# Performance work log

Measured on AMD Instinct MI355X. Metric: run time of the kernel, lower is better.

## Reference

```python
import jax, jax.numpy as jnp
import numpy as np


def setup_inputs() -> dict:
    key = jax.random.key(0)
    kq, kk, kv = jax.random.split(key, 3)
    B, Nq, Nk, d = 16, 4096, 4096, 128
    return {
        "query": jax.random.normal(kq, (B, Nq, d), dtype=jnp.float32),
        "key": jax.random.normal(kk, (B, Nk, d), dtype=jnp.float32),
        "value": jax.random.normal(kv, (B, Nk, d), dtype=jnp.float32),
    }


def reference(query, key, value):
    # weights = softmax(QK^T / sqrt(d)) with causal mask; dropout p=0.0 is identity
    d = key.shape[-1]
    scale = 1.0 / jnp.sqrt(jnp.asarray(d, dtype=query.dtype))
    scores = jnp.einsum("bqd,bkd->bqk", query, key) * scale  # [B, Nq, Nk]
    Nq, Nk = scores.shape[-2], scores.shape[-1]
    causal = jnp.tril(jnp.ones((Nq, Nk), dtype=bool))
    scores = jnp.where(causal, scores, jnp.asarray(-jnp.inf, dtype=scores.dtype))
    weights = jax.nn.softmax(scores, axis=-1)
    return jnp.einsum("bqk,bkv->bqv", weights, value)
```

## Files before the change

kernel.cpp:

```cpp
#include <hip/hip_runtime.h>
#include <stdint.h>


#define NB 16
#define NS 4096
#define DH 128

typedef float          fx4   __attribute__((ext_vector_type(4)));
typedef uint32_t       ux4   __attribute__((ext_vector_type(4)));
typedef __bf16         bfv8  __attribute__((ext_vector_type(8)));
typedef __bf16         bfv4  __attribute__((ext_vector_type(4)));
typedef unsigned short u16x4 __attribute__((ext_vector_type(4)));

typedef const uint32_t __attribute__((address_space(1))) glob_u32;
typedef uint32_t       __attribute__((address_space(3))) lds_u32;

__device__ __forceinline__ fx4 mfma16(bfv8 a, bfv8 b, fx4 c) {
  return __builtin_amdgcn_mfma_f32_16x16x32_bf16(a, b, c, 0, 0, 0);
}

__global__ void __launch_bounds__(256) prepack_kernel(
    const float* __restrict__ K, const float* __restrict__ V,
    unsigned short* __restrict__ Kf, unsigned short* __restrict__ Vf) {
  __shared__ __align__(16) unsigned short tile[64][136];
  const int bid = blockIdx.x;
  const int b = bid >> 6, kvblk = bid & 63;
  const int kvb = kvblk << 6;
  const int tid = threadIdx.x;
  const size_t fbase = ((size_t)(b * 64 + kvblk)) * 8192;

  {
    const int tt = tid >> 6, lane = tid & 63;
    const int ln16 = lane & 15, g = lane >> 4;
    const float* kp = K + (((size_t)(b * NS + kvb + 16 * tt + ln16)) << 7) + 8 * g;
    unsigned short* op = Kf + fbase + tt * 2048 + lane * 8;
#pragma unroll
    for (int c = 0; c < 4; ++c) {
      fx4 a0 = *(const fx4*)(kp + 32 * c);
      fx4 a1 = *(const fx4*)(kp + 32 * c + 4);
      bfv8 t;
#pragma unroll
      for (int j = 0; j < 4; ++j) {
        t[j]     = (__bf16)a0[j];
        t[j + 4] = (__bf16)a1[j];
      }
      *(ux4*)(op + c * 512) = __builtin_bit_cast(ux4, t);
    }
  }

  {
    const int r = tid >> 2, cq = tid & 3;
    const float* vp = V + (((size_t)(b * NS + kvb + r)) << 7) + 32 * cq;
#pragma unroll
    for (int h = 0; h < 4; ++h) {
      fx4 f0 = *(const fx4*)(vp + 8 * h);
      fx4 f1 = *(const fx4*)(vp + 8 * h + 4);
      bfv8 t;
#pragma unroll
      for (int j = 0; j < 4; ++j) {
        t[j]     = (__bf16)f0[j];
        t[j + 4] = (__bf16)f1[j];
      }
      *(ux4*)&tile[r][32 * cq + 8 * h] = __builtin_bit_cast(ux4, t);
    }
  }
  __syncthreads();
  {
    const int dt = tid >> 5, c = (tid >> 4) & 1, ln16 = tid & 15;
    const int d = 16 * dt + ln16;
    unsigned short* op = Vf + fbase + c * 4096 + dt * 512 + ln16 * 8;
#pragma unroll
    for (int g = 0; g < 4; ++g) {
      unsigned short e[8];
#pragma unroll
      for (int j = 0; j < 4; ++j) {
        e[j]     = tile[32 * c + 4 * g + j][d];
        e[j + 4] = tile[32 * c + 16 + 4 * g + j][d];
      }
      *(ux4*)(op + g * 128) = *(const ux4*)e;
    }
  }
}

__global__ void __launch_bounds__(512, 4) attn_kernel(
    const float* __restrict__ Q, const unsigned short* __restrict__ Kf,
    const unsigned short* __restrict__ Vf, float* __restrict__ O,
    unsigned short* __restrict__ Pa, float* __restrict__ Ml, int split) {
  __shared__ __align__(16) unsigned char sm[32768];

  const int wid  = blockIdx.x;
  const int tid  = threadIdx.x;
  const int w    = tid >> 6;
  const int lane = tid & 63;
  const int g    = lane >> 4;
  const int ln16 = lane & 15;

  int b, t, u0, un, mode;
  int t1 = 0, u1b = 0;
  int again = 0;

  if (split) {
    const int piece = wid >> 8;
    const int v     = (wid >> 4) & 15;
    b = wid & 15;
    t = 31 - v;
    if (piece == 0) {
      u0 = 0; un = 66; mode = 1;
    } else {
      u0 = 66; un = 128 - 4 * v; mode = 2;
      t1 = v; u1b = 4 * v + 4; again = 1;
    }
  } else {
    const int half = wid >> 8, ii = wid & 255;
    b = ii & 15;
    const int qi = ii >> 4;
    t = half ? qi : 31 - qi;
    u0 = 0; un = 4 * t + 4; mode = 0;
  }

  const float SCALE = 0.12753102f;
  const fx4 z4 = {0.f, 0.f, 0.f, 0.f};

  const unsigned char* kfB = (const unsigned char*)Kf + (size_t)b * 1048576;
  const unsigned char* vfB = (const unsigned char*)Vf + (size_t)b * 1048576;

#define STAGE(jb, bo)                                                         \
  do {                                                                        \
    const unsigned char* gk = kfB + (size_t)(jb) * 8192;                      \
    const unsigned char* gv = vfB + (size_t)(jb) * 8192;                      \
    __builtin_amdgcn_global_load_lds((glob_u32*)(gk + w * 1024 + lane * 16),  \
                                     (lds_u32*)(sm + (bo) + w * 1024), 16, 0, 0); \
    __builtin_amdgcn_global_load_lds((glob_u32*)(gv + w * 1024 + lane * 16),  \
                                     (lds_u32*)(sm + (bo) + 8192 + w * 1024), 16, 0, 0); \
  } while (0)

  for (;;) {
    const int qw = (t << 7) + 16 * w;

    bfv8 qf[4];
#pragma unroll
    for (int c = 0; c < 4; ++c) {
      const float* qp = Q + (((size_t)(b * NS + qw + ln16)) << 7) + 32 * c + 8 * g;
      fx4 a0 = *(const fx4*)qp;
      fx4 a1 = *(const fx4*)(qp + 4);
      bfv8 tt_;
#pragma unroll
      for (int j = 0; j < 4; ++j) {
        tt_[j]     = (__bf16)(a0[j] * SCALE);
        tt_[j + 4] = (__bf16)(a1[j] * SCALE);
      }
      qf[c] = tt_;
    }

    fx4 acc[8];
#pragma unroll
    for (int dt = 0; dt < 8; ++dt) acc[dt] = z4;
    float mrun = -1e30f;
    float lsum = 0.f;

    const int nkvw = (qw >> 5) + 1;
    const int qrow = qw + ln16;

    STAGE(u0, 0);
    asm volatile("s_waitcnt vmcnt(0)" ::: "memory");
    __builtin_amdgcn_s_barrier();
    asm volatile("" ::: "memory");

    int cur = 0;
    for (int jb = u0; jb < un; ++jb) {
      if (jb + 1 < un) STAGE(jb + 1, (cur ^ 1) * 16384);

      if (jb < nkvw) {
        const unsigned char* kb = sm + cur * 16384;
        const unsigned char* vb = kb + 8192;

        fx4 s[2];
        s[0] = z4; s[1] = z4;
        __builtin_amdgcn_s_setprio(1);
#pragma unroll
        for (int tt = 0; tt < 2; ++tt) {
#pragma unroll
          for (int c = 0; c < 4; ++c) {
            bfv8 kfr = *(const bfv8*)(kb + tt * 4096 + c * 1024 + lane * 16);
            s[tt] = mfma16(kfr, qf[c], s[tt]);
          }
        }
        __builtin_amdgcn_s_setprio(0);

        const int kvb = jb << 5;
        if (kvb + 31 > qrow - ln16 + 0 + (qw - qw) + qw - qw + qw % 1 + 31 * 0 + (qw & 0) ? (kvb + 31 > qw) : 0) {  }
        if (kvb + 31 > qw) {
#pragma unroll
          for (int tt = 0; tt < 2; ++tt)
#pragma unroll
            for (int r = 0; r < 4; ++r) {
              int kvpos = kvb + 16 * tt + 4 * g + r;
              if (kvpos > qrow) s[tt][r] = -1e30f;
            }
        }

        fx4 m4 = __builtin_elementwise_max(s[0], s[1]);
        float pm = fmaxf(fmaxf(m4[0], m4[1]), fmaxf(m4[2], m4[3]));
        pm = fmaxf(pm, __shfl_xor(pm, 16));
        pm = fmaxf(pm, __shfl_xor(pm, 32));
        if (__any(pm > mrun + 8.0f)) {
          float mn = fmaxf(mrun, pm);
          float f  = __builtin_amdgcn_exp2f(mrun - mn);
          lsum *= f;
#pragma unroll
          for (int dt = 0; dt < 8; ++dt) acc[dt] *= f;
          mrun = mn;
        }
#pragma unroll
        for (int tt = 0; tt < 2; ++tt)
#pragma unroll
          for (int r = 0; r < 4; ++r)
            s[tt][r] = __builtin_amdgcn_exp2f(s[tt][r] - mrun);
        fx4 r4 = s[0] + s[1];
        float rs = (r4[0] + r4[1]) + (r4[2] + r4[3]);
        rs += __shfl_xor(rs, 16);
        rs += __shfl_xor(rs, 32);
        lsum += rs;
        bfv8 pb;
#pragma unroll
        for (int j = 0; j < 4; ++j) {
          pb[j]     = (__bf16)s[0][j];
          pb[j + 4] = (__bf16)s[1][j];
        }

        __builtin_amdgcn_s_setprio(1);
#pragma unroll
        for (int dt = 0; dt < 8; ++dt) {
          bfv8 vfr = *(const bfv8*)(vb + dt * 1024 + lane * 16);
          acc[dt] = mfma16(vfr, pb, acc[dt]);
        }
        __builtin_amdgcn_s_setprio(0);
      }

      asm volatile("s_waitcnt vmcnt(0)" ::: "memory");
      __builtin_amdgcn_s_barrier();
      asm volatile("" ::: "memory");
      cur ^= 1;
    }

    if (mode == 0) {
      float inv = 1.0f / lsum;
      float* ob = O + (((size_t)(b * NS + qrow)) << 7) + 4 * g;
#pragma unroll
      for (int dt = 0; dt < 8; ++dt) *(fx4*)(ob + 16 * dt) = acc[dt] * inv;
    } else {
      if (mode == 1) {
        float* ob = O + (((size_t)(b * NS + qrow)) << 7) + 4 * g;
#pragma unroll
        for (int dt = 0; dt < 8; ++dt) *(fx4*)(ob + 16 * dt) = acc[dt];
      } else {
        const int row = 16 * w + ln16;
        unsigned short* pp =
            Pa + (((size_t)((b * 16 + (t - 16)) * 128 + row)) << 7) + 4 * g;
#pragma unroll
        for (int dt = 0; dt < 8; ++dt) {
          bfv4 t4;
#pragma unroll
          for (int j = 0; j < 4; ++j) t4[j] = (__bf16)acc[dt][j];
          *(u16x4*)(pp + 16 * dt) = __builtin_bit_cast(u16x4, t4);
        }
      }
      if (g == 0) {
        const int slot = mode - 1;
        const int row = 16 * w + ln16;
        float* mlp = Ml + (size_t)(((b * 16 + (t - 16)) * 2 + slot) * 2) * 128;
        mlp[row]       = mrun;
        mlp[128 + row] = lsum;
      }
    }

    if (!again) break;
    again = 0;
    t = t1; u0 = 0; un = u1b; mode = 0;
  }
#undef STAGE
}

__global__ void __launch_bounds__(256) merge_kernel(
    float* __restrict__ O, const unsigned short* __restrict__ Pa,
    const float* __restrict__ Ml) {
  const int gid = blockIdx.x * 256 + threadIdx.x;
  const int d4  = gid & 31;
  const int rg  = gid >> 5;
  const int b   = rg >> 11;
  const int r2  = rg & 2047;
  const int tt  = r2 >> 7;
  const int row = r2 & 127;

  const float* mlp = Ml + (size_t)((b * 16 + tt) * 4) * 128;
  const float m1 = mlp[row],       l1 = mlp[128 + row];
  const float m2 = mlp[256 + row], l2 = mlp[384 + row];
  const float m  = fmaxf(m1, m2);
  const float w1 = __builtin_amdgcn_exp2f(m1 - m);
  const float w2 = __builtin_amdgcn_exp2f(m2 - m);

  float* op = O + (((size_t)(b * NS + (16 + tt) * 128 + row)) << 7) + 4 * d4;
  fx4 a1 = *(const fx4*)op;
  const unsigned short* pp =
      Pa + (((size_t)((b * 16 + tt) * 128 + row)) << 7) + 4 * d4;
  bfv4 a2b = __builtin_bit_cast(bfv4, *(const u16x4*)pp);
  fx4 a2;
#pragma unroll
  for (int j = 0; j < 4; ++j) a2[j] = (float)a2b[j];

  const float inv = 1.0f / (w1 * l1 + w2 * l2);
  fx4 o = (a1 * w1 + a2 * w2) * inv;
  *(fx4*)op = o;
}

extern "C" void kernel_launch(void* const* d_in, const int* in_sizes, int n_in,
                              void* d_out, int out_size, void* d_ws, size_t ws_size,
                              hipStream_t stream) {
  (void)in_sizes; (void)n_in; (void)out_size;
  const float* Q = (const float*)d_in[0];
  const float* K = (const float*)d_in[1];
  const float* V = (const float*)d_in[2];
  float* O = (float*)d_out;

  unsigned short* Kf = (unsigned short*)d_ws;
  unsigned short* Vf = Kf + (size_t)NB * NS * DH;
  unsigned short* Pa = (unsigned short*)((char*)d_ws + 33554432);
  float*          Ml = (float*)((char*)d_ws + 41943040);

  const size_t NEED = 41943040 + 524288;
  const int split = (ws_size >= NEED) ? 1 : 0;

  prepack_kernel<<<dim3(NB * 64), dim3(256), 0, stream>>>(K, V, Kf, Vf);
  attn_kernel<<<dim3(512), dim3(512), 0, stream>>>(Q, Kf, Vf, O, Pa, Ml, split);
  if (split) merge_kernel<<<dim3(4096), dim3(256), 0, stream>>>(O, Pa, Ml);
}
```

Baseline: 124.5 us.

## Give each wave two query tiles and stage four KV blocks per barrier

The block drops from 8 to 4 waves, and each wave now handles 32 query rows as two 16-row tiles, so every K/V fragment read from LDS feeds two MFMAs. K/V staging now loads four 32-key blocks per batch into 64KB of LDS, paying one barrier and wait per four blocks instead of one per block. The split point of the two-piece split changes from 66 to 64. In exchange, register pressure roughly doubles, fewer waves are resident, and the load is no longer overlapped with compute: each batch waits for all four blocks to arrive.

```diff
diff --git a/kernel.cpp b/kernel.cpp
--- a/kernel.cpp
+++ b/kernel.cpp
@@ -82,11 +82,11 @@
   }
 }
 
-__global__ void __launch_bounds__(512, 4) attn_kernel(
+__global__ void __launch_bounds__(256, 2) attn_kernel(
     const float* __restrict__ Q, const unsigned short* __restrict__ Kf,
     const unsigned short* __restrict__ Vf, float* __restrict__ O,
     unsigned short* __restrict__ Pa, float* __restrict__ Ml, int split) {
-  __shared__ __align__(16) unsigned char sm[32768];
+  __shared__ __align__(16) unsigned char sm[65536];
 
   const int wid  = blockIdx.x;
   const int tid  = threadIdx.x;
@@ -96,18 +96,17 @@
   const int ln16 = lane & 15;
 
   int b, t, u0, un, mode;
-  int t1 = 0, u1b = 0;
-  int again = 0;
+  int t1 = 0, u1b = 0, again = 0;
 
   if (split) {
-    const int piece = wid >> 8;
-    const int v     = (wid >> 4) & 15;
+    const int half = wid >> 8;
+    const int v    = (wid >> 4) & 15;
     b = wid & 15;
     t = 31 - v;
-    if (piece == 0) {
-      u0 = 0; un = 66; mode = 1;
+    if (half == 0) {
+      u0 = 0; un = 64; mode = 1;
     } else {
-      u0 = 66; un = 128 - 4 * v; mode = 2;
+      u0 = 64; un = 128 - 4 * v; mode = 2;
       t1 = v; u1b = 4 * v + 4; again = 1;
     }
   } else {
@@ -124,153 +123,198 @@
   const unsigned char* kfB = (const unsigned char*)Kf + (size_t)b * 1048576;
   const unsigned char* vfB = (const unsigned char*)Vf + (size_t)b * 1048576;
 
-#define STAGE(jb, bo)                                                         \
-  do {                                                                        \
-    const unsigned char* gk = kfB + (size_t)(jb) * 8192;                      \
-    const unsigned char* gv = vfB + (size_t)(jb) * 8192;                      \
-    __builtin_amdgcn_global_load_lds((glob_u32*)(gk + w * 1024 + lane * 16),  \
-                                     (lds_u32*)(sm + (bo) + w * 1024), 16, 0, 0); \
-    __builtin_amdgcn_global_load_lds((glob_u32*)(gv + w * 1024 + lane * 16),  \
-                                     (lds_u32*)(sm + (bo) + 8192 + w * 1024), 16, 0, 0); \
+#define STAGE(jb, so)                                                          \
+  do {                                                                         \
+    const unsigned char* gk = kfB + (size_t)(jb) * 8192;                       \
+    const unsigned char* gv = vfB + (size_t)(jb) * 8192;                       \
+    __builtin_amdgcn_global_load_lds((glob_u32*)(gk + w * 2048 + lane * 16),   \
+        (lds_u32*)(sm + (so) + w * 2048), 16, 0, 0);                           \
+    __builtin_amdgcn_global_load_lds((glob_u32*)(gk + w * 2048 + 1024 + lane * 16), \
+        (lds_u32*)(sm + (so) + w * 2048 + 1024), 16, 0, 0);                    \
+    __builtin_amdgcn_global_load_lds((glob_u32*)(gv + w * 2048 + lane * 16),   \
+        (lds_u32*)(sm + (so) + 8192 + w * 2048), 16, 0, 0);                    \
+    __builtin_amdgcn_global_load_lds((glob_u32*)(gv + w * 2048 + 1024 + lane * 16), \
+        (lds_u32*)(sm + (so) + 8192 + w * 2048 + 1024), 16, 0, 0);             \
   } while (0)
 
+#define COMPUTE(jb, so)                                                        \
+  do {                                                                         \
+    const unsigned char* kb = sm + (so);                                       \
+    const unsigned char* vb = kb + 8192;                                       \
+    fx4 s[2][2];                                                               \
+    s[0][0] = z4; s[0][1] = z4; s[1][0] = z4; s[1][1] = z4;                    \
+    __builtin_amdgcn_s_setprio(1);                                             \
+    _Pragma("unroll")                                                          \
+    for (int tt = 0; tt < 2; ++tt) {                                           \
+      _Pragma("unroll")                                                        \
+      for (int c = 0; c < 4; ++c) {                                            \
+        bfv8 kfr = *(const bfv8*)(kb + tt * 4096 + c * 1024 + lane * 16);      \
+        s[0][tt] = mfma16(kfr, qf[0][c], s[0][tt]);                            \
+        s[1][tt] = mfma16(kfr, qf[1][c], s[1][tt]);                            \
+      }                                                                        \
+    }                                                                          \
+    __builtin_amdgcn_s_setprio(0);                                             \
+    const int kvb = (jb) << 5;                                                 \
+    if (kvb + 31 > qw) {                                                       \
+      _Pragma("unroll")                                                        \
+      for (int qt = 0; qt < 2; ++qt) {                                         \
+        const int qrow = qw + qt * 16 + ln16;                                  \
+        _Pragma("unroll")                                                      \
+        for (int tt = 0; tt < 2; ++tt)                                         \
+          _Pragma("unroll")                                                    \
+          for (int r = 0; r < 4; ++r) {                                        \
+            int kvpos = kvb + 16 * tt + 4 * g + r;                             \
+            if (kvpos > qrow) s[qt][tt][r] = -1e30f;                           \
+          }                                                                    \
+      }                                                                        \
+    }                                                                          \
+    bfv8 pb[2];                                                                \
+    _Pragma("unroll")                                                          \
+    for (int qt = 0; qt < 2; ++qt) {                                           \
+      fx4 m4 = __builtin_elementwise_max(s[qt][0], s[qt][1]);                  \
+      float pm = fmaxf(fmaxf(m4[0], m4[1]), fmaxf(m4[2], m4[3]));              \
+      pm = fmaxf(pm, __shfl_xor(pm, 16));                                      \
+      pm = fmaxf(pm, __shfl_xor(pm, 32));                                      \
+      if (__any(pm > mrun[qt] + 8.0f)) {                                       \
+        float mn = fmaxf(mrun[qt], pm);                                        \
+        float f  = __builtin_amdgcn_exp2f(mrun[qt] - mn);                      \
+        lsum[qt] *= f;                                                         \
+        _Pragma("unroll")                                                      \
+        for (int dt = 0; dt < 8; ++dt) acc[qt][dt] *= f;                       \
+        mrun[qt] = mn;                                                         \
+      }                                                                        \
+      _Pragma("unroll")                                                        \
+      for (int tt = 0; tt < 2; ++tt)                                           \
+        _Pragma("unroll")                                                      \
+        for (int r = 0; r < 4; ++r)                                            \
+          s[qt][tt][r] = __builtin_amdgcn_exp2f(s[qt][tt][r] - mrun[qt]);      \
+      fx4 r4 = s[qt][0] + s[qt][1];                                            \
+      float rs = (r4[0] + r4[1]) + (r4[2] + r4[3]);                            \
+      rs += __shfl_xor(rs, 16);                                                \
+      rs += __shfl_xor(rs, 32);                                                \
+      lsum[qt] += rs;                                                          \
+      bfv8 tt_;                                                                \
+      _Pragma("unroll")                                                        \
+      for (int j = 0; j < 4; ++j) {                                            \
+        tt_[j]     = (__bf16)s[qt][0][j];                                      \
+        tt_[j + 4] = (__bf16)s[qt][1][j];                                      \
+      }                                                                        \
+      pb[qt] = tt_;                                                            \
+    }                                                                          \
+    __builtin_amdgcn_s_setprio(1);                                             \
+    _Pragma("unroll")                                                          \
+    for (int dt = 0; dt < 8; ++dt) {                                           \
+      bfv8 vfr = *(const bfv8*)(vb + dt * 1024 + lane * 16);                   \
+      acc[0][dt] = mfma16(vfr, pb[0], acc[0][dt]);                             \
+      acc[1][dt] = mfma16(vfr, pb[1], acc[1][dt]);                             \
+    }                                                                          \
+    __builtin_amdgcn_s_setprio(0);                                             \
+  } while (0)
+
   for (;;) {
-    const int qw = (t << 7) + 16 * w;
-
-    bfv8 qf[4];
-#pragma unroll
-    for (int c = 0; c < 4; ++c) {
-      const float* qp = Q + (((size_t)(b * NS + qw + ln16)) << 7) + 32 * c + 8 * g;
-      fx4 a0 = *(const fx4*)qp;
-      fx4 a1 = *(const fx4*)(qp + 4);
-      bfv8 tt_;
-#pragma unroll
-      for (int j = 0; j < 4; ++j) {
-        tt_[j]     = (__bf16)(a0[j] * SCALE);
-        tt_[j + 4] = (__bf16)(a1[j] * SCALE);
-      }
-      qf[c] = tt_;
-    }
-
-    fx4 acc[8];
-#pragma unroll
-    for (int dt = 0; dt < 8; ++dt) acc[dt] = z4;
-    float mrun = -1e30f;
-    float lsum = 0.f;
+    const int qw = (t << 7) + 32 * w;
+
+    bfv8 qf[2][4];
+#pragma unroll
+    for (int qt = 0; qt < 2; ++qt) {
+#pragma unroll
+      for (int c = 0; c < 4; ++c) {
+        const float* qp = Q + (((size_t)(b * NS + qw + qt * 16 + ln16)) << 7) + 32 * c + 8 * g;
+        fx4 a0 = *(const fx4*)qp;
+        fx4 a1 = *(const fx4*)(qp + 4);
+        bfv8 tt_;
+#pragma unroll
+        for (int j = 0; j < 4; ++j) {
+          tt_[j]     = (__bf16)(a0[j] * SCALE);
+          tt_[j + 4] = (__bf16)(a1[j] * SCALE);
+        }
+        qf[qt][c] = tt_;
+      }
+    }
+
+    fx4 acc[2][8];
+#pragma unroll
+    for (int qt = 0; qt < 2; ++qt)
+#pragma unroll
+      for (int dt = 0; dt < 8; ++dt) acc[qt][dt] = z4;
+    float mrun[2] = {-1e30f, -1e30f};
+    float lsum[2] = {0.f, 0.f};
 
     const int nkvw = (qw >> 5) + 1;
-    const int qrow = qw + ln16;
-
-    STAGE(u0, 0);
+
+    STAGE(u0 + 0, 0);
+    STAGE(u0 + 1, 16384);
+    STAGE(u0 + 2, 32768);
+    STAGE(u0 + 3, 49152);
     asm volatile("s_waitcnt vmcnt(0)" ::: "memory");
     __builtin_amdgcn_s_barrier();
     asm volatile("" ::: "memory");
 
-    int cur = 0;
-    for (int jb = u0; jb < un; ++jb) {
-      if (jb + 1 < un) STAGE(jb + 1, (cur ^ 1) * 16384);
-
-      if (jb < nkvw) {
-        const unsigned char* kb = sm + cur * 16384;
-        const unsigned char* vb = kb + 8192;
-
-        fx4 s[2];
-        s[0] = z4; s[1] = z4;
-        __builtin_amdgcn_s_setprio(1);
-#pragma unroll
-        for (int tt = 0; tt < 2; ++tt) {
-#pragma unroll
-          for (int c = 0; c < 4; ++c) {
-            bfv8 kfr = *(const bfv8*)(kb + tt * 4096 + c * 1024 + lane * 16);
-            s[tt] = mfma16(kfr, qf[c], s[tt]);
+    for (int base = u0; base < un; base += 4) {
+      if (base + 4 <= nkvw) {
+        COMPUTE(base + 0, 0);
+        COMPUTE(base + 1, 16384);
+        COMPUTE(base + 2, 32768);
+        COMPUTE(base + 3, 49152);
+      } else {
+        if (base + 0 < nkvw) COMPUTE(base + 0, 0);
+        if (base + 1 < nkvw) COMPUTE(base + 1, 16384);
+        if (base + 2 < nkvw) COMPUTE(base + 2, 32768);
+        if (base + 3 < nkvw) COMPUTE(base + 3, 49152);
+      }
+      asm volatile("" ::: "memory");
+      __builtin_amdgcn_s_barrier();
+      if (base + 4 < un) {
+        STAGE(base + 4, 0);
+        STAGE(base + 5, 16384);
+        STAGE(base + 6, 32768);
+        STAGE(base + 7, 49152);
+        asm volatile("s_waitcnt vmcnt(0)" ::: "memory");
+      }
+      __builtin_amdgcn_s_barrier();
+      asm volatile("" ::: "memory");
+    }
+
+    if (mode == 0) {
+#pragma unroll
+      for (int qt = 0; qt < 2; ++qt) {
+        float inv = 1.0f / lsum[qt];
+        float* ob = O + (((size_t)(b * NS + qw + qt * 16 + ln16)) << 7) + 4 * g;
+#pragma unroll
+        for (int dt = 0; dt < 8; ++dt) *(fx4*)(ob + 16 * dt) = acc[qt][dt] * inv;
+      }
+    } else {
+      if (mode == 1) {
+#pragma unroll
+        for (int qt = 0; qt < 2; ++qt) {
+          float* ob = O + (((size_t)(b * NS + qw + qt * 16 + ln16)) << 7) + 4 * g;
+#pragma unroll
+          for (int dt = 0; dt < 8; ++dt) *(fx4*)(ob + 16 * dt) = acc[qt][dt];
+        }
+      } else {
+#pragma unroll
+        for (int qt = 0; qt < 2; ++qt) {
+          const int row = 32 * w + 16 * qt + ln16;
+          unsigned short* pp =
+              Pa + (((size_t)((b * 16 + (t - 16)) * 128 + row)) << 7) + 4 * g;
+#pragma unroll
+          for (int dt = 0; dt < 8; ++dt) {
+            bfv4 t4;
+#pragma unroll
+            for (int j = 0; j < 4; ++j) t4[j] = (__bf16)acc[qt][dt][j];
+            *(u16x4*)(pp + 16 * dt) = __builtin_bit_cast(u16x4, t4);
           }
         }
-        __builtin_amdgcn_s_setprio(0);
-
-        const int kvb = jb << 5;
-        if (kvb + 31 > qrow - ln16 + 0 + (qw - qw) + qw - qw + qw % 1 + 31 * 0 + (qw & 0) ? (kvb + 31 > qw) : 0) {  }
-        if (kvb + 31 > qw) {
-#pragma unroll
-          for (int tt = 0; tt < 2; ++tt)
-#pragma unroll
-            for (int r = 0; r < 4; ++r) {
-              int kvpos = kvb + 16 * tt + 4 * g + r;
-              if (kvpos > qrow) s[tt][r] = -1e30f;
-            }
-        }
-
-        fx4 m4 = __builtin_elementwise_max(s[0], s[1]);
-        float pm = fmaxf(fmaxf(m4[0], m4[1]), fmaxf(m4[2], m4[3]));
-        pm = fmaxf(pm, __shfl_xor(pm, 16));
-        pm = fmaxf(pm, __shfl_xor(pm, 32));
-        if (__any(pm > mrun + 8.0f)) {
-          float mn = fmaxf(mrun, pm);
-          float f  = __builtin_amdgcn_exp2f(mrun - mn);
-          lsum *= f;
-#pragma unroll
-          for (int dt = 0; dt < 8; ++dt) acc[dt] *= f;
-          mrun = mn;
-        }
-#pragma unroll
-        for (int tt = 0; tt < 2; ++tt)
-#pragma unroll
-          for (int r = 0; r < 4; ++r)
-            s[tt][r] = __builtin_amdgcn_exp2f(s[tt][r] - mrun);
-        fx4 r4 = s[0] + s[1];
-        float rs = (r4[0] + r4[1]) + (r4[2] + r4[3]);
-        rs += __shfl_xor(rs, 16);
-        rs += __shfl_xor(rs, 32);
-        lsum += rs;
-        bfv8 pb;
-#pragma unroll
-        for (int j = 0; j < 4; ++j) {
-          pb[j]     = (__bf16)s[0][j];
-          pb[j + 4] = (__bf16)s[1][j];
-        }
-
-        __builtin_amdgcn_s_setprio(1);
-#pragma unroll
-        for (int dt = 0; dt < 8; ++dt) {
-          bfv8 vfr = *(const bfv8*)(vb + dt * 1024 + lane * 16);
-          acc[dt] = mfma16(vfr, pb, acc[dt]);
-        }
-        __builtin_amdgcn_s_setprio(0);
-      }
-
-      asm volatile("s_waitcnt vmcnt(0)" ::: "memory");
-      __builtin_amdgcn_s_barrier();
-      asm volatile("" ::: "memory");
-      cur ^= 1;
-    }
-
-    if (mode == 0) {
-      float inv = 1.0f / lsum;
-      float* ob = O + (((size_t)(b * NS + qrow)) << 7) + 4 * g;
-#pragma unroll
-      for (int dt = 0; dt < 8; ++dt) *(fx4*)(ob + 16 * dt) = acc[dt] * inv;
-    } else {
-      if (mode == 1) {
-        float* ob = O + (((size_t)(b * NS + qrow)) << 7) + 4 * g;
-#pragma unroll
-        for (int dt = 0; dt < 8; ++dt) *(fx4*)(ob + 16 * dt) = acc[dt];
-      } else {
-        const int row = 16 * w + ln16;
-        unsigned short* pp =
-            Pa + (((size_t)((b * 16 + (t - 16)) * 128 + row)) << 7) + 4 * g;
-#pragma unroll
-        for (int dt = 0; dt < 8; ++dt) {
-          bfv4 t4;
-#pragma unroll
-          for (int j = 0; j < 4; ++j) t4[j] = (__bf16)acc[dt][j];
-          *(u16x4*)(pp + 16 * dt) = __builtin_bit_cast(u16x4, t4);
-        }
       }
       if (g == 0) {
         const int slot = mode - 1;
-        const int row = 16 * w + ln16;
         float* mlp = Ml + (size_t)(((b * 16 + (t - 16)) * 2 + slot) * 2) * 128;
-        mlp[row]       = mrun;
-        mlp[128 + row] = lsum;
+#pragma unroll
+        for (int qt = 0; qt < 2; ++qt) {
+          const int row = 32 * w + 16 * qt + ln16;
+          mlp[row]       = mrun[qt];
+          mlp[128 + row] = lsum[qt];
+        }
       }
     }
 
@@ -278,6 +322,7 @@
     again = 0;
     t = t1; u0 = 0; un = u1b; mode = 0;
   }
+#undef COMPUTE
 #undef STAGE
 }
 
@@ -331,6 +376,6 @@
   const int split = (ws_size >= NEED) ? 1 : 0;
 
   prepack_kernel<<<dim3(NB * 64), dim3(256), 0, stream>>>(K, V, Kf, Vf);
-  attn_kernel<<<dim3(512), dim3(512), 0, stream>>>(Q, Kf, Vf, O, Pa, Ml, split);
+  attn_kernel<<<dim3(512), dim3(256), 0, stream>>>(Q, Kf, Vf, O, Pa, Ml, split);
   if (split) merge_kernel<<<dim3(4096), dim3(256), 0, stream>>>(O, Pa, Ml);
 }
```

New measurement: 128.8 us. 3.5% more time.
